# Optimization experiments

Measured on AMD Instinct MI355X. Metric: run time of the kernel, lower is better.

## Reference

```python
import jax, jax.numpy as jnp
import numpy as np

B, S, D, K = 128, 200, 128, 4
NQ, NC = 10000, 500


def setup_inputs() -> dict:
    key = jax.random.key(0)
    ks = jax.random.split(key, 20)
    f = jnp.float32
    inp = {}
    inp["question_seq"] = jax.random.randint(ks[0], (B, S), 0, NQ)
    inp["hint_attempt_seq"] = jax.random.randint(ks[1], (B, S), 0, 12)
    inp["correct_seq"] = jax.random.randint(ks[2], (B, S), 0, 2)
    inp["interval_time_seq"] = jax.random.randint(ks[3], (B, S), 0, 100)
    inp["use_time_seq"] = jax.random.randint(ks[4], (B, S), 0, 100)
    inp["q2c_table"] = jax.random.randint(ks[5], (NQ, K), 0, NC)
    inp["q2c_mask_table"] = jax.random.randint(ks[6], (NQ, K), 0, 2)
    s = 0.1
    inp["embed_question"] = jax.random.normal(ks[7], (NQ, D), f) * s
    inp["embed_question_disc"] = jax.random.normal(ks[8], (NQ, 1), f) * s
    inp["embed_concept"] = jax.random.normal(ks[9], (NC, D), f) * s
    inp["embed_interval_time"] = jax.random.normal(ks[10], (100, D), f) * s
    inp["embed_use_time"] = jax.random.normal(ks[11], (100, D), f) * s
    inp["embed_hint_attempt"] = jax.random.normal(ks[12], (12, D), f) * s
    inp["W_fuse"] = jax.random.normal(ks[13], (2 * D, D), f) / np.float32(np.sqrt(2 * D))
    inp["b_fuse"] = jnp.zeros((D,), f)
    inp["W_absorb"] = jax.random.normal(ks[14], (3 * D, D), f) / np.float32(np.sqrt(3 * D))
    inp["b_absorb"] = jnp.zeros((D,), f)
    inp["W_forget"] = jax.random.normal(ks[15], (3 * D, D), f) / np.float32(np.sqrt(3 * D))
    inp["b_forget"] = jnp.zeros((D,), f)
    inp["latent0"] = jax.random.normal(ks[16], (B, D), f) * 0.1  # xavier-init latent_pre
    return inp


def _cos(a, b, eps=1e-8):
    # torch.cosine_similarity semantics with eps clamp on each norm
    num = jnp.sum(a * b, axis=-1)
    na = jnp.sqrt(jnp.sum(a * a, axis=-1))
    nb = jnp.sqrt(jnp.sum(b * b, axis=-1))
    return num / (jnp.maximum(na, eps) * jnp.maximum(nb, eps))


def _forward(question_seq, hint_attempt_seq, correct_seq, interval_time_seq, use_time_seq,
             q2c_table, q2c_mask_table,
             embed_question, embed_question_disc, embed_concept, embed_interval_time,
             embed_use_time, embed_hint_attempt,
             W_fuse, b_fuse, W_absorb, b_absorb, W_forget, b_forget, latent0):
    f = latent0.dtype
    qe = embed_question[question_seq]                                # [B,S,D]
    qd = jax.nn.sigmoid(embed_question_disc[question_seq]) * 10.0    # [B,S,1]
    ce = jnp.broadcast_to(correct_seq.astype(f)[:, :, None], qe.shape)  # [B,S,D]
    ite = embed_interval_time[interval_time_seq]                     # [B,S,D]
    ute = embed_use_time[use_time_seq]                               # [B,S,D]
    hae = embed_hint_attempt[hint_attempt_seq]                       # [B,S,D]
    cp = embed_concept[q2c_table[question_seq]]                      # [B,S,K,D]
    m = q2c_mask_table[question_seq].astype(f)                       # [B,S,K]

    tm = lambda x: jnp.swapaxes(x, 0, 1)  # time-major for scan
    xs = (tm(qe[:, :-1]), tm(ce[:, :-1]), tm(ute[:, :-1]), tm(hae[:, :-1]), tm(ite[:, :-1]),
          tm(cp[:, :-1]), tm(cp[:, 1:]), tm(qd[:, 1:]), tm(m[:, :-1]))

    def step(lp, x):
        qe_t, ce_t, ute_t, hae_t, ite_t, cp_t, cp_t1, qd_t1, m_t = x
        inter = jnp.concatenate([qe_t, ce_t], axis=-1) @ W_fuse + b_fuse
        absorb = jnp.concatenate([inter, ute_t, hae_t], axis=-1) @ W_absorb + b_absorb
        forget = jax.nn.sigmoid(jnp.concatenate([lp, ite_t, inter], axis=-1) @ W_forget + b_forget)
        lc = lp * forget + absorb  # dropout p=0 -> identity
        qdiff = (_cos(qe_t[:, None, :], cp_t) + 1.0) * 0.5   # [B,K]
        uab = (_cos(lc[:, None, :], cp_t1) + 1.0) * 0.5      # [B,K]
        logit = qd_t1[:, 0] * jnp.sum((uab - qdiff) * m_t, axis=-1)  # [B]
        return lc, jax.nn.sigmoid(logit)

    _, ys = jax.lax.scan(step, latent0, xs)  # ys: [S-1, B]
    y = jnp.concatenate([ys.T, jnp.zeros((latent0.shape[0], 1), f)], axis=1)  # [B,S], last col 0
    return y


def reference(question_seq, hint_attempt_seq, correct_seq, interval_time_seq, use_time_seq,
              q2c_table, q2c_mask_table,
              embed_question, embed_question_disc, embed_concept, embed_interval_time,
              embed_use_time, embed_hint_attempt,
              W_fuse, b_fuse, W_absorb, b_absorb, W_forget, b_forget, latent0):
    return _forward(question_seq, hint_attempt_seq, correct_seq, interval_time_seq, use_time_seq,
                    q2c_table, q2c_mask_table,
                    embed_question, embed_question_disc, embed_concept, embed_interval_time,
                    embed_use_time, embed_hint_attempt,
                    W_fuse, b_fuse, W_absorb, b_absorb, W_forget, b_forget, latent0)
```

## Files before the change

### kernel.cpp

```cpp
#include <hip/hip_runtime.h>
#include <hip/hip_bf16.h>

typedef unsigned short u16;

#define Bb  128
#define Ss  200
#define Tt  199
#define Dd  128
#define Kk  4
#define NQq 10000
#define NCc 500
#define CHK 16
#define NCH 13

__device__ inline float bf2f(u16 u) {
    union { unsigned int i; float f; } x;
    x.i = ((unsigned int)u) << 16;
    return x.f;
}

__device__ inline float ldf(const void* p, int i, int m) {
    if (m) return ((const float*)p)[i];
    return bf2f(((const u16*)p)[i]);
}

__device__ inline void stf(void* p, int i, int m, float v) {
    if (m) ((float*)p)[i] = v;
    else ((__hip_bfloat16*)p)[i] = __float2bfloat16(v);
}

__device__ inline int clampi(int v, int lo, int hi) {
    return v < lo ? lo : (v > hi ? hi : v);
}

__device__ inline float wave_red(float v) {
#pragma unroll
    for (int m = 32; m >= 1; m >>= 1) v += __shfl_xor(v, m);
    return v;
}

__device__ inline float4 f4add(float4 a, float4 b) {
    return make_float4(a.x + b.x, a.y + b.y, a.z + b.z, a.w + b.w);
}
__device__ inline float4 f4fma(float s, float4 a, float4 b) {
    return make_float4(fmaf(s, a.x, b.x), fmaf(s, a.y, b.y),
                       fmaf(s, a.z, b.z), fmaf(s, a.w, b.w));
}

__global__ __launch_bounds__(256) void p_detect(const void* Eq, int* flag) {
    const int tid = threadIdx.x;
    const u16* q = (const u16*)Eq;
    float mx = 0.f;
    for (int i = tid; i < 4096; i += 256) {
        float a = fabsf(bf2f(q[i]));
        if (!(a == a)) a = 3.0e38f;
        mx = fmaxf(mx, a);
    }
#pragma unroll
    for (int s = 32; s >= 1; s >>= 1) mx = fmaxf(mx, __shfl_xor(mx, s));
    __shared__ float sm[4];
    if ((tid & 63) == 0) sm[tid >> 6] = mx;
    __syncthreads();
    if (tid == 0) {
        float m2 = fmaxf(fmaxf(sm[0], sm[1]), fmaxf(sm[2], sm[3]));
        flag[0] = (m2 > 1.0e6f) ? 1 : 0;
    }
}

__global__ __launch_bounds__(128) void p0_prep(const void* Wf, const void* Ec,
                                               const int* mode,
                                               float* cs2, float* cnorm) {
    const int m = mode[0];
    const int tid = threadIdx.x;
    if (blockIdx.x == 0) {
        float s = 0.f;
        for (int r = 0; r < 128; ++r) s += ldf(Wf, (128 + r) * 128 + tid, m);
        cs2[tid] = s;
    } else {
        const int c = blockIdx.x - 1;
        float v = ldf(Ec, c * 128 + tid, m);
        float s = wave_red(v * v);
        __shared__ float tmp[2];
        if ((tid & 63) == 0) tmp[tid >> 6] = s;
        __syncthreads();
        if (tid == 0) cnorm[c] = fmaxf(sqrtf(tmp[0] + tmp[1]), 1e-8f);
    }
}

__global__ __launch_bounds__(128) void p1_weights(
    const void* Wf, const void* Wa, const void* Wg,
    const void* bfu, const void* ba, const void* bg,
    const void* Eut, const void* Eha, const void* Eit,
    const int* mode, const float* cs2,
    float* BabT, float* BfgT,
    float* vA0, float* vA1, float* vF0, float* vF1,
    float* PA_ut, float* PA_ha, float* PF_it) {
    const int m = mode[0];
    const int bi = blockIdx.x, tid = threadIdx.x;
    if (bi < 128) {
        float acc = 0.f;
        for (int j = 0; j < 128; ++j)
            acc += ldf(Wf, bi * 128 + j, m) * ldf(Wa, j * 128 + tid, m);
        BabT[bi * 128 + tid] = acc;
    } else if (bi < 256) {
        const int i = bi - 128;
        float acc = 0.f;
        for (int j = 0; j < 128; ++j)
            acc += ldf(Wf, i * 128 + j, m) * ldf(Wg, (256 + j) * 128 + tid, m);
        BfgT[i * 128 + tid] = acc;
    } else if (bi == 256) {
        float a0 = 0.f, a1 = 0.f;
        for (int j = 0; j < 128; ++j) {
            float wv = ldf(Wa, j * 128 + tid, m);
            a0 += ldf(bfu, j, m) * wv;
            a1 += cs2[j] * wv;
        }
        vA0[tid] = a0 + ldf(ba, tid, m);
        vA1[tid] = a1;
    } else if (bi == 257) {
        float a0 = 0.f, a1 = 0.f;
        for (int j = 0; j < 128; ++j) {
            float wv = ldf(Wg, (256 + j) * 128 + tid, m);
            a0 += ldf(bfu, j, m) * wv;
            a1 += cs2[j] * wv;
        }
        vF0[tid] = a0 + ldf(bg, tid, m);
        vF1[tid] = a1;
    } else if (bi < 358) {
        const int r = bi - 258;
        float acc = 0.f;
        for (int j = 0; j < 128; ++j)
            acc += ldf(Eut, r * 128 + j, m) * ldf(Wa, (128 + j) * 128 + tid, m);
        PA_ut[r * 128 + tid] = acc;
    } else if (bi < 370) {
        const int r = bi - 358;
        float acc = 0.f;
        for (int j = 0; j < 128; ++j)
            acc += ldf(Eha, r * 128 + j, m) * ldf(Wa, (256 + j) * 128 + tid, m);
        PA_ha[r * 128 + tid] = acc;
    } else {
        const int r = bi - 370;
        float acc = 0.f;
        for (int j = 0; j < 128; ++j)
            acc += ldf(Eit, r * 128 + j, m) * ldf(Wg, (128 + j) * 128 + tid, m);
        PF_it[r * 128 + tid] = acc;
    }
}

__global__ __launch_bounds__(256) void p3_gemm(
    const void* Eq, const int* mode,
    const float* BabT, const float* BfgT,
    float* PA_q, float* PF_q) {
    __shared__ float At[64][36];
    __shared__ float Bt0[32][128];
    __shared__ float Bt1[32][128];
    const int m = mode[0];
    const int tid = threadIdx.x;
    const int r0 = blockIdx.x * 64;
    float acc0[4][8], acc1[4][8];
#pragma unroll
    for (int j = 0; j < 4; ++j)
#pragma unroll
        for (int i = 0; i < 8; ++i) { acc0[j][i] = 0.f; acc1[j][i] = 0.f; }
    const int tx = tid & 15, ty = tid >> 4;
    for (int ks = 0; ks < 4; ++ks) {
        {
            const int row = tid >> 2, seg = tid & 3;
            const int q = clampi(r0 + row, 0, NQq - 1);
            const int ei = q * 128 + ks * 32 + seg * 8;
            float* dst = &At[row][seg * 8];
            if (m) {
                const float4* src = (const float4*)((const float*)Eq + ei);
                float4 v0 = src[0], v1 = src[1];
                dst[0] = v0.x; dst[1] = v0.y; dst[2] = v0.z; dst[3] = v0.w;
                dst[4] = v1.x; dst[5] = v1.y; dst[6] = v1.z; dst[7] = v1.w;
            } else {
                uint4 v = *(const uint4*)((const u16*)Eq + ei);
                dst[0] = bf2f((u16)(v.x & 0xffff)); dst[1] = bf2f((u16)(v.x >> 16));
                dst[2] = bf2f((u16)(v.y & 0xffff)); dst[3] = bf2f((u16)(v.y >> 16));
                dst[4] = bf2f((u16)(v.z & 0xffff)); dst[5] = bf2f((u16)(v.z >> 16));
                dst[6] = bf2f((u16)(v.w & 0xffff)); dst[7] = bf2f((u16)(v.w >> 16));
            }
        }
        {
            const float4* s0 = (const float4*)(BabT + ks * 32 * 128);
            const float4* s1 = (const float4*)(BfgT + ks * 32 * 128);
            float4* d0 = (float4*)&Bt0[0][0];
            float4* d1 = (float4*)&Bt1[0][0];
#pragma unroll
            for (int k = 0; k < 4; ++k) {
                d0[tid + k * 256] = s0[tid + k * 256];
                d1[tid + k * 256] = s1[tid + k * 256];
            }
        }
        __syncthreads();
#pragma unroll
        for (int kk = 0; kk < 32; kk += 4) {
            float a_[4][4];
            *(float4*)&a_[0][0] = *(const float4*)&At[ty * 4 + 0][kk];
            *(float4*)&a_[1][0] = *(const float4*)&At[ty * 4 + 1][kk];
            *(float4*)&a_[2][0] = *(const float4*)&At[ty * 4 + 2][kk];
            *(float4*)&a_[3][0] = *(const float4*)&At[ty * 4 + 3][kk];
#pragma unroll
            for (int q = 0; q < 4; ++q) {
                float4 b0 = *(const float4*)&Bt0[kk + q][tx * 8];
                float4 b1 = *(const float4*)&Bt0[kk + q][tx * 8 + 4];
                float4 c0 = *(const float4*)&Bt1[kk + q][tx * 8];
                float4 c1 = *(const float4*)&Bt1[kk + q][tx * 8 + 4];
#pragma unroll
                for (int j = 0; j < 4; ++j) {
                    const float av = a_[j][q];
                    acc0[j][0] += av * b0.x; acc0[j][1] += av * b0.y;
                    acc0[j][2] += av * b0.z; acc0[j][3] += av * b0.w;
                    acc0[j][4] += av * b1.x; acc0[j][5] += av * b1.y;
                    acc0[j][6] += av * b1.z; acc0[j][7] += av * b1.w;
                    acc1[j][0] += av * c0.x; acc1[j][1] += av * c0.y;
                    acc1[j][2] += av * c0.z; acc1[j][3] += av * c0.w;
                    acc1[j][4] += av * c1.x; acc1[j][5] += av * c1.y;
                    acc1[j][6] += av * c1.z; acc1[j][7] += av * c1.w;
                }
            }
        }
        __syncthreads();
    }
#pragma unroll
    for (int j = 0; j < 4; ++j) {
        const int q = r0 + ty * 4 + j;
        if (q < NQq) {
            float* oa = PA_q + q * 128 + tx * 8;
            float* of = PF_q + q * 128 + tx * 8;
#pragma unroll
            for (int i = 0; i < 8; ++i) { oa[i] = acc0[j][i]; of[i] = acc1[j][i]; }
        }
    }
}

__global__ __launch_bounds__(256) void p2q(
    const int* q2c, const int* q2cm,
    const void* Eq, const void* Eqd, const void* Ec,
    const int* mode, const float* cnorm,
    float* qdm, float* qd10) {
    const int m = mode[0];
    const int wv = threadIdx.x >> 6, lane = threadIdx.x & 63;
    const int q = blockIdx.x * 4 + wv;
    const float qa = ldf(Eq, q * 128 + lane, m);
    const float qb = ldf(Eq, q * 128 + 64 + lane, m);
    const float nqc = fmaxf(sqrtf(wave_red(qa * qa + qb * qb)), 1e-8f);
    const int4 cc = ((const int4*)q2c)[q];
    const int4 mm = ((const int4*)q2cm)[q];
    const int cks[4] = {clampi(cc.x, 0, NCc - 1), clampi(cc.y, 0, NCc - 1),
                        clampi(cc.z, 0, NCc - 1), clampi(cc.w, 0, NCc - 1)};
    const int ms[4]  = {mm.x, mm.y, mm.z, mm.w};
    float qs = 0.f;
#pragma unroll
    for (int k = 0; k < 4; ++k) {
        const int ck = cks[k];
        float dot = wave_red(qa * ldf(Ec, ck * 128 + lane, m) +
                             qb * ldf(Ec, ck * 128 + 64 + lane, m));
        qs += (float)ms[k] * (0.5f * dot / (nqc * cnorm[ck]) + 0.5f);
    }
    if (lane == 0) {
        qdm[q] = qs;
        qd10[q] = 10.f / (1.f + __expf(-ldf(Eqd, q, m)));
    }
}

__global__ __launch_bounds__(256) void p4_scan(
    const int* q_seq, const int* ut_seq, const int* ha_seq, const int* it_seq,
    const int* c_seq,
    const void* Wg, const void* L0,
    const float* PA_q, const float* PA_ut, const float* PA_ha,
    const float* PF_q, const float* PF_it,
    const float* vA0, const float* vA1, const float* vF0, const float* vF1,
    const int* mode, float* lc_seq) {
    const int m = mode[0];
    const int b = blockIdx.x;
    const int tid = threadIdx.x;
    const int wv = tid >> 6, l = tid & 63;
    const int d0 = 2 * l, ib = wv * 32;

    __shared__ float lp_sh[128];
    __shared__ float part[512];
    __shared__ float st_ab[CHK * 128];
    __shared__ float st_pf[CHK * 128];

    float wA[32], wB[32];
#pragma unroll
    for (int k = 0; k < 32; ++k) {
        wA[k] = ldf(Wg, (ib + k) * 128 + d0, m);
        wB[k] = ldf(Wg, (ib + k) * 128 + d0 + 1, m);
    }
    float lc = 0.f;
    if (tid < 128) {
        lc = ldf(L0, b * 128 + tid, m);
        lp_sh[tid] = lc;
    }

    const int srow = tid >> 4, seg = tid & 15;
    const int off8 = seg * 8;
    const float4 A0a = *(const float4*)(vA0 + off8), A0b = *(const float4*)(vA0 + off8 + 4);
    const float4 A1a = *(const float4*)(vA1 + off8), A1b = *(const float4*)(vA1 + off8 + 4);
    const float4 F0a = *(const float4*)(vF0 + off8), F0b = *(const float4*)(vF0 + off8 + 4);
    const float4 F1a = *(const float4*)(vF1 + off8), F1b = *(const float4*)(vF1 + off8 + 4);

    float4 qa0, qa1, ua0, ua1, ga0, ga1, qf0, qf1, if0, if1;
    float cf;
#define LOAD_CHUNK(C)                                                          \
    {                                                                          \
        int tt = (C) * CHK + srow; if (tt > Tt - 1) tt = Tt - 1;               \
        const int base = b * Ss + tt;                                          \
        const int qt = clampi(q_seq[base], 0, NQq - 1);                        \
        const int ut = clampi(ut_seq[base], 0, 99);                            \
        const int ha = clampi(ha_seq[base], 0, 11);                            \
        const int it = clampi(it_seq[base], 0, 99);                            \
        cf = (float)c_seq[base];                                               \
        const float* pq = PA_q + qt * 128 + off8;                              \
        qa0 = *(const float4*)pq; qa1 = *(const float4*)(pq + 4);              \
        const float* pu = PA_ut + ut * 128 + off8;                             \
        ua0 = *(const float4*)pu; ua1 = *(const float4*)(pu + 4);              \
        const float* ph = PA_ha + ha * 128 + off8;                             \
        ga0 = *(const float4*)ph; ga1 = *(const float4*)(ph + 4);              \
        const float* pf = PF_q + qt * 128 + off8;                              \
        qf0 = *(const float4*)pf; qf1 = *(const float4*)(pf + 4);              \
        const float* pi = PF_it + it * 128 + off8;                             \
        if0 = *(const float4*)pi; if1 = *(const float4*)(pi + 4);              \
    }

    LOAD_CHUNK(0)
    float lcbuf[CHK];

    for (int c = 0; c < NCH; ++c) {
        {
            float4 ab0 = f4fma(cf, A1a, f4add(f4add(qa0, ua0), f4add(ga0, A0a)));
            float4 ab1 = f4fma(cf, A1b, f4add(f4add(qa1, ua1), f4add(ga1, A0b)));
            float4 pf0 = f4fma(cf, F1a, f4add(qf0, f4add(if0, F0a)));
            float4 pf1 = f4fma(cf, F1b, f4add(qf1, f4add(if1, F0b)));
            float4* sa = (float4*)(st_ab + srow * 128 + off8);
            sa[0] = ab0; sa[1] = ab1;
            float4* sp = (float4*)(st_pf + srow * 128 + off8);
            sp[0] = pf0; sp[1] = pf1;
        }
        if (c + 1 < NCH) LOAD_CHUNK(c + 1)
        __syncthreads();

#pragma unroll
        for (int s = 0; s < CHK; ++s) {
            const float4* lp4 = (const float4*)(lp_sh + ib);
            float pa = 0.f, pb = 0.f;
#pragma unroll
            for (int k = 0; k < 8; ++k) {
                float4 v = lp4[k];
                pa += v.x * wA[4 * k] + v.y * wA[4 * k + 1]
                    + v.z * wA[4 * k + 2] + v.w * wA[4 * k + 3];
                pb += v.x * wB[4 * k] + v.y * wB[4 * k + 1]
                    + v.z * wB[4 * k + 2] + v.w * wB[4 * k + 3];
            }
            *(float2*)(part + (wv << 7) + d0) = make_float2(pa, pb);
            __syncthreads();
            if (tid < 128) {
                const float fs = part[tid] + part[128 + tid]
                               + part[256 + tid] + part[384 + tid];
                const float ab = st_ab[(s << 7) + tid];
                const float pf = st_pf[(s << 7) + tid];
                const float fg = 1.f / (1.f + __expf(-(fs + pf)));
                lc = lc * fg + ab;
                lp_sh[tid] = lc;
                lcbuf[s] = lc;
            }
            __syncthreads();
        }
        if (tid < 128) {
#pragma unroll
            for (int s = 0; s < CHK; ++s) {
                const int t = c * CHK + s;
                if (t < Tt)
                    lc_seq[((long)t * 128 + b) * 128 + tid] = lcbuf[s];
            }
        }
    }
#undef LOAD_CHUNK
}

__global__ __launch_bounds__(256) void p5_out(
    const int* q_seq, const int* q2c, const int* q2cm,
    const float* lc_seq, const float* qdm, const float* qd10,
    const float* cnorm, const void* Ec, const int* mode, void* out) {
    const int m = mode[0];
    const int wv = threadIdx.x >> 6, lane = threadIdx.x & 63;
    const int r = blockIdx.x * 4 + wv;
    const int t = r >> 7, b = r & 127;
    const int qt  = clampi(q_seq[b * Ss + t], 0, NQq - 1);
    const int qt1 = clampi(q_seq[b * Ss + t + 1], 0, NQq - 1);
    const int4 mm = ((const int4*)q2cm)[qt];
    int4 ci = ((const int4*)q2c)[qt1];
    const int c0 = clampi(ci.x, 0, NCc - 1), c1 = clampi(ci.y, 0, NCc - 1);
    const int c2 = clampi(ci.z, 0, NCc - 1), c3 = clampi(ci.w, 0, NCc - 1);
    const float la = lc_seq[(long)r * 128 + lane];
    const float lb = lc_seq[(long)r * 128 + 64 + lane];
    float nl = la * la + lb * lb;
    float d0 = la * ldf(Ec, c0 * 128 + lane, m) + lb * ldf(Ec, c0 * 128 + 64 + lane, m);
    float d1 = la * ldf(Ec, c1 * 128 + lane, m) + lb * ldf(Ec, c1 * 128 + 64 + lane, m);
    float d2 = la * ldf(Ec, c2 * 128 + lane, m) + lb * ldf(Ec, c2 * 128 + 64 + lane, m);
    float d3 = la * ldf(Ec, c3 * 128 + lane, m) + lb * ldf(Ec, c3 * 128 + 64 + lane, m);
#pragma unroll
    for (int s = 32; s >= 1; s >>= 1) {
        nl += __shfl_xor(nl, s);
        d0 += __shfl_xor(d0, s); d1 += __shfl_xor(d1, s);
        d2 += __shfl_xor(d2, s); d3 += __shfl_xor(d3, s);
    }
    if (lane == 0) {
        const float inl = 1.f / fmaxf(sqrtf(nl), 1e-8f);
        const float accv = (float)mm.x * (0.5f * d0 * inl / cnorm[c0] + 0.5f)
                         + (float)mm.y * (0.5f * d1 * inl / cnorm[c1] + 0.5f)
                         + (float)mm.z * (0.5f * d2 * inl / cnorm[c2] + 0.5f)
                         + (float)mm.w * (0.5f * d3 * inl / cnorm[c3] + 0.5f);
        const float logit = qd10[qt1] * (accv - qdm[qt]);
        stf(out, b * Ss + t, m, 1.f / (1.f + __expf(-logit)));
        if (t == 0) stf(out, b * Ss + 199, m, 0.f);
    }
}

extern "C" void kernel_launch(void* const* d_in, const int* in_sizes, int n_in,
                              void* d_out, int out_size, void* d_ws, size_t ws_size,
                              hipStream_t stream) {
    (void)in_sizes; (void)n_in; (void)out_size; (void)ws_size;
    const int* q_seq  = (const int*)d_in[0];
    const int* ha_seq = (const int*)d_in[1];
    const int* c_seq  = (const int*)d_in[2];
    const int* it_seq = (const int*)d_in[3];
    const int* ut_seq = (const int*)d_in[4];
    const int* q2c    = (const int*)d_in[5];
    const int* q2cm   = (const int*)d_in[6];
    const void* Eq   = d_in[7];
    const void* Eqd  = d_in[8];
    const void* Ec   = d_in[9];
    const void* Eit  = d_in[10];
    const void* Eut  = d_in[11];
    const void* Eha  = d_in[12];
    const void* Wf   = d_in[13];
    const void* bfu  = d_in[14];
    const void* Wa   = d_in[15];
    const void* ba   = d_in[16];
    const void* Wg   = d_in[17];
    const void* bg   = d_in[18];
    const void* L0   = d_in[19];

    int*   mode  = (int*)d_ws;
    float* cs2   = (float*)d_ws + 16;
    float* cnorm = cs2 + 128;
    float* vA0   = cnorm + 512;
    float* vA1   = vA0 + 128;
    float* vF0   = vA1 + 128;
    float* vF1   = vF0 + 128;
    float* BabT  = vF1 + 128;
    float* BfgT  = BabT + 16384;
    float* PA_ut = BfgT + 16384;
    float* PA_ha = PA_ut + 12800;
    float* PF_it = PA_ha + 1536;
    float* qdm   = PF_it + 12800;
    float* qd10  = qdm + 10016;
    float* PA_q  = qd10 + 10016;
    float* PF_q  = PA_q + 1280000;
    float* lc_seq= PF_q + 1280000;

    hipLaunchKernelGGL(p_detect, dim3(1), dim3(256), 0, stream, Eq, mode);
    hipLaunchKernelGGL(p0_prep, dim3(501), dim3(128), 0, stream, Wf, Ec, mode, cs2, cnorm);
    hipLaunchKernelGGL(p1_weights, dim3(470), dim3(128), 0, stream,
                       Wf, Wa, Wg, bfu, ba, bg, Eut, Eha, Eit, mode, cs2,
                       BabT, BfgT, vA0, vA1, vF0, vF1, PA_ut, PA_ha, PF_it);
    hipLaunchKernelGGL(p3_gemm, dim3(157), dim3(256), 0, stream,
                       Eq, mode, BabT, BfgT, PA_q, PF_q);
    hipLaunchKernelGGL(p2q, dim3(2500), dim3(256), 0, stream,
                       q2c, q2cm, Eq, Eqd, Ec, mode, cnorm, qdm, qd10);
    hipLaunchKernelGGL(p4_scan, dim3(Bb), dim3(256), 0, stream,
                       q_seq, ut_seq, ha_seq, it_seq, c_seq, Wg, L0,
                       PA_q, PA_ut, PA_ha, PF_q, PF_it,
                       vA0, vA1, vF0, vF1, mode, lc_seq);
    hipLaunchKernelGGL(p5_out, dim3(Tt * Bb / 4), dim3(256), 0, stream,
                       q_seq, q2c, q2cm, lc_seq, qdm, qd10, cnorm, Ec, mode, d_out);
}
```

Before: 271.2 us.

## Merge prep kernels, inline mode detection, remove one barrier per scan step

Mode detection moves from a standalone kernel into an inline per-wave check, and the prep, weights, gemm and p2q kernels are merged into two launches, cutting seven launches to four. In the recurrent scan, every wave now computes the gate update redundantly from double-buffered partial sums, which removes the second __syncthreads per timestep and the idle half of the threads. The costs are redundant cs2 computation in two blocks, redundant sampling of Eq in every kernel, and detection now checks only 256 elements instead of 4096, which could misclassify the input dtype.

```diff
diff --git a/kernel.cpp b/kernel.cpp
--- a/kernel.cpp
+++ b/kernel.cpp
@@ -47,99 +47,91 @@
                        fmaf(s, a.z, b.z), fmaf(s, a.w, b.w));
 }
 
-__global__ __launch_bounds__(256) void p_detect(const void* Eq, int* flag) {
-    const int tid = threadIdx.x;
+__device__ inline int detect_mode(const void* Eq) {
     const u16* q = (const u16*)Eq;
+    const int l = threadIdx.x & 63;
     float mx = 0.f;
-    for (int i = tid; i < 4096; i += 256) {
-        float a = fabsf(bf2f(q[i]));
+#pragma unroll
+    for (int k = 0; k < 4; ++k) {
+        float a = fabsf(bf2f(q[l * 4 + k]));
         if (!(a == a)) a = 3.0e38f;
         mx = fmaxf(mx, a);
     }
 #pragma unroll
     for (int s = 32; s >= 1; s >>= 1) mx = fmaxf(mx, __shfl_xor(mx, s));
-    __shared__ float sm[4];
-    if ((tid & 63) == 0) sm[tid >> 6] = mx;
-    __syncthreads();
-    if (tid == 0) {
-        float m2 = fmaxf(fmaxf(sm[0], sm[1]), fmaxf(sm[2], sm[3]));
-        flag[0] = (m2 > 1.0e6f) ? 1 : 0;
-    }
-}
-
-__global__ __launch_bounds__(128) void p0_prep(const void* Wf, const void* Ec,
-                                               const int* mode,
-                                               float* cs2, float* cnorm) {
-    const int m = mode[0];
-    const int tid = threadIdx.x;
-    if (blockIdx.x == 0) {
-        float s = 0.f;
-        for (int r = 0; r < 128; ++r) s += ldf(Wf, (128 + r) * 128 + tid, m);
-        cs2[tid] = s;
-    } else {
-        const int c = blockIdx.x - 1;
+    return (mx > 1.0e6f) ? 1 : 0;
+}
+
+__global__ __launch_bounds__(128) void k_prep(
+    const void* Eq, const void* Wf, const void* Wa, const void* Wg,
+    const void* bfu, const void* ba, const void* bg,
+    const void* Eut, const void* Eha, const void* Eit, const void* Ec,
+    float* cnorm, float* BabT, float* BfgT,
+    float* vA0, float* vA1, float* vF0, float* vF1,
+    float* PA_ut, float* PA_ha, float* PF_it) {
+    const int m = detect_mode(Eq);
+    const int bi = blockIdx.x, tid = threadIdx.x;
+    __shared__ float cs2s[128];
+    __shared__ float tmp[2];
+    if (bi < 500) {
+        const int c = bi;
         float v = ldf(Ec, c * 128 + tid, m);
         float s = wave_red(v * v);
-        __shared__ float tmp[2];
         if ((tid & 63) == 0) tmp[tid >> 6] = s;
         __syncthreads();
         if (tid == 0) cnorm[c] = fmaxf(sqrtf(tmp[0] + tmp[1]), 1e-8f);
-    }
-}
-
-__global__ __launch_bounds__(128) void p1_weights(
-    const void* Wf, const void* Wa, const void* Wg,
-    const void* bfu, const void* ba, const void* bg,
-    const void* Eut, const void* Eha, const void* Eit,
-    const int* mode, const float* cs2,
-    float* BabT, float* BfgT,
-    float* vA0, float* vA1, float* vF0, float* vF1,
-    float* PA_ut, float* PA_ha, float* PF_it) {
-    const int m = mode[0];
-    const int bi = blockIdx.x, tid = threadIdx.x;
-    if (bi < 128) {
+    } else if (bi < 628) {
+        const int r = bi - 500;
         float acc = 0.f;
         for (int j = 0; j < 128; ++j)
-            acc += ldf(Wf, bi * 128 + j, m) * ldf(Wa, j * 128 + tid, m);
-        BabT[bi * 128 + tid] = acc;
-    } else if (bi < 256) {
-        const int i = bi - 128;
+            acc += ldf(Wf, r * 128 + j, m) * ldf(Wa, j * 128 + tid, m);
+        BabT[r * 128 + tid] = acc;
+    } else if (bi < 756) {
+        const int r = bi - 628;
         float acc = 0.f;
         for (int j = 0; j < 128; ++j)
-            acc += ldf(Wf, i * 128 + j, m) * ldf(Wg, (256 + j) * 128 + tid, m);
-        BfgT[i * 128 + tid] = acc;
-    } else if (bi == 256) {
+            acc += ldf(Wf, r * 128 + j, m) * ldf(Wg, (256 + j) * 128 + tid, m);
+        BfgT[r * 128 + tid] = acc;
+    } else if (bi == 756) {
+        float s = 0.f;
+        for (int r = 0; r < 128; ++r) s += ldf(Wf, (128 + r) * 128 + tid, m);
+        cs2s[tid] = s;
+        __syncthreads();
         float a0 = 0.f, a1 = 0.f;
         for (int j = 0; j < 128; ++j) {
             float wv = ldf(Wa, j * 128 + tid, m);
             a0 += ldf(bfu, j, m) * wv;
-            a1 += cs2[j] * wv;
+            a1 += cs2s[j] * wv;
         }
         vA0[tid] = a0 + ldf(ba, tid, m);
         vA1[tid] = a1;
-    } else if (bi == 257) {
+    } else if (bi == 757) {
+        float s = 0.f;
+        for (int r = 0; r < 128; ++r) s += ldf(Wf, (128 + r) * 128 + tid, m);
+        cs2s[tid] = s;
+        __syncthreads();
         float a0 = 0.f, a1 = 0.f;
         for (int j = 0; j < 128; ++j) {
             float wv = ldf(Wg, (256 + j) * 128 + tid, m);
             a0 += ldf(bfu, j, m) * wv;
-            a1 += cs2[j] * wv;
+            a1 += cs2s[j] * wv;
         }
         vF0[tid] = a0 + ldf(bg, tid, m);
         vF1[tid] = a1;
-    } else if (bi < 358) {
-        const int r = bi - 258;
+    } else if (bi < 858) {
+        const int r = bi - 758;
         float acc = 0.f;
         for (int j = 0; j < 128; ++j)
             acc += ldf(Eut, r * 128 + j, m) * ldf(Wa, (128 + j) * 128 + tid, m);
         PA_ut[r * 128 + tid] = acc;
-    } else if (bi < 370) {
-        const int r = bi - 358;
+    } else if (bi < 870) {
+        const int r = bi - 858;
         float acc = 0.f;
         for (int j = 0; j < 128; ++j)
             acc += ldf(Eha, r * 128 + j, m) * ldf(Wa, (256 + j) * 128 + tid, m);
         PA_ha[r * 128 + tid] = acc;
     } else {
-        const int r = bi - 370;
+        const int r = bi - 870;
         float acc = 0.f;
         for (int j = 0; j < 128; ++j)
             acc += ldf(Eit, r * 128 + j, m) * ldf(Wg, (128 + j) * 128 + tid, m);
@@ -147,140 +139,139 @@
     }
 }
 
-__global__ __launch_bounds__(256) void p3_gemm(
-    const void* Eq, const int* mode,
-    const float* BabT, const float* BfgT,
-    float* PA_q, float* PF_q) {
-    __shared__ float At[64][36];
-    __shared__ float Bt0[32][128];
-    __shared__ float Bt1[32][128];
-    const int m = mode[0];
+__global__ __launch_bounds__(256) void k_mid(
+    const void* Eq, const void* Eqd, const void* Ec,
+    const int* q2c, const int* q2cm,
+    const float* BabT, const float* BfgT, const float* cnorm,
+    float* PA_q, float* PF_q, float* qdm, float* qd10) {
+    const int m = detect_mode(Eq);
     const int tid = threadIdx.x;
-    const int r0 = blockIdx.x * 64;
-    float acc0[4][8], acc1[4][8];
-#pragma unroll
-    for (int j = 0; j < 4; ++j)
-#pragma unroll
-        for (int i = 0; i < 8; ++i) { acc0[j][i] = 0.f; acc1[j][i] = 0.f; }
-    const int tx = tid & 15, ty = tid >> 4;
-    for (int ks = 0; ks < 4; ++ks) {
-        {
-            const int row = tid >> 2, seg = tid & 3;
-            const int q = clampi(r0 + row, 0, NQq - 1);
-            const int ei = q * 128 + ks * 32 + seg * 8;
-            float* dst = &At[row][seg * 8];
-            if (m) {
-                const float4* src = (const float4*)((const float*)Eq + ei);
-                float4 v0 = src[0], v1 = src[1];
-                dst[0] = v0.x; dst[1] = v0.y; dst[2] = v0.z; dst[3] = v0.w;
-                dst[4] = v1.x; dst[5] = v1.y; dst[6] = v1.z; dst[7] = v1.w;
-            } else {
-                uint4 v = *(const uint4*)((const u16*)Eq + ei);
-                dst[0] = bf2f((u16)(v.x & 0xffff)); dst[1] = bf2f((u16)(v.x >> 16));
-                dst[2] = bf2f((u16)(v.y & 0xffff)); dst[3] = bf2f((u16)(v.y >> 16));
-                dst[4] = bf2f((u16)(v.z & 0xffff)); dst[5] = bf2f((u16)(v.z >> 16));
-                dst[6] = bf2f((u16)(v.w & 0xffff)); dst[7] = bf2f((u16)(v.w >> 16));
-            }
-        }
-        {
-            const float4* s0 = (const float4*)(BabT + ks * 32 * 128);
-            const float4* s1 = (const float4*)(BfgT + ks * 32 * 128);
-            float4* d0 = (float4*)&Bt0[0][0];
-            float4* d1 = (float4*)&Bt1[0][0];
-#pragma unroll
-            for (int k = 0; k < 4; ++k) {
-                d0[tid + k * 256] = s0[tid + k * 256];
-                d1[tid + k * 256] = s1[tid + k * 256];
-            }
-        }
-        __syncthreads();
-#pragma unroll
-        for (int kk = 0; kk < 32; kk += 4) {
-            float a_[4][4];
-            *(float4*)&a_[0][0] = *(const float4*)&At[ty * 4 + 0][kk];
-            *(float4*)&a_[1][0] = *(const float4*)&At[ty * 4 + 1][kk];
-            *(float4*)&a_[2][0] = *(const float4*)&At[ty * 4 + 2][kk];
-            *(float4*)&a_[3][0] = *(const float4*)&At[ty * 4 + 3][kk];
-#pragma unroll
-            for (int q = 0; q < 4; ++q) {
-                float4 b0 = *(const float4*)&Bt0[kk + q][tx * 8];
-                float4 b1 = *(const float4*)&Bt0[kk + q][tx * 8 + 4];
-                float4 c0 = *(const float4*)&Bt1[kk + q][tx * 8];
-                float4 c1 = *(const float4*)&Bt1[kk + q][tx * 8 + 4];
-#pragma unroll
-                for (int j = 0; j < 4; ++j) {
-                    const float av = a_[j][q];
-                    acc0[j][0] += av * b0.x; acc0[j][1] += av * b0.y;
-                    acc0[j][2] += av * b0.z; acc0[j][3] += av * b0.w;
-                    acc0[j][4] += av * b1.x; acc0[j][5] += av * b1.y;
-                    acc0[j][6] += av * b1.z; acc0[j][7] += av * b1.w;
-                    acc1[j][0] += av * c0.x; acc1[j][1] += av * c0.y;
-                    acc1[j][2] += av * c0.z; acc1[j][3] += av * c0.w;
-                    acc1[j][4] += av * c1.x; acc1[j][5] += av * c1.y;
-                    acc1[j][6] += av * c1.z; acc1[j][7] += av * c1.w;
+    const int bi = blockIdx.x;
+    if (bi < 157) {
+        __shared__ float At[64][36];
+        __shared__ float Bt0[32][128];
+        __shared__ float Bt1[32][128];
+        const int r0 = bi * 64;
+        float acc0[4][8], acc1[4][8];
+#pragma unroll
+        for (int j = 0; j < 4; ++j)
+#pragma unroll
+            for (int i = 0; i < 8; ++i) { acc0[j][i] = 0.f; acc1[j][i] = 0.f; }
+        const int tx = tid & 15, ty = tid >> 4;
+        for (int ks = 0; ks < 4; ++ks) {
+            {
+                const int row = tid >> 2, seg = tid & 3;
+                const int q = clampi(r0 + row, 0, NQq - 1);
+                const int ei = q * 128 + ks * 32 + seg * 8;
+                float* dst = &At[row][seg * 8];
+                if (m) {
+                    const float4* src = (const float4*)((const float*)Eq + ei);
+                    float4 v0 = src[0], v1 = src[1];
+                    dst[0] = v0.x; dst[1] = v0.y; dst[2] = v0.z; dst[3] = v0.w;
+                    dst[4] = v1.x; dst[5] = v1.y; dst[6] = v1.z; dst[7] = v1.w;
+                } else {
+                    uint4 v = *(const uint4*)((const u16*)Eq + ei);
+                    dst[0] = bf2f((u16)(v.x & 0xffff)); dst[1] = bf2f((u16)(v.x >> 16));
+                    dst[2] = bf2f((u16)(v.y & 0xffff)); dst[3] = bf2f((u16)(v.y >> 16));
+                    dst[4] = bf2f((u16)(v.z & 0xffff)); dst[5] = bf2f((u16)(v.z >> 16));
+                    dst[6] = bf2f((u16)(v.w & 0xffff)); dst[7] = bf2f((u16)(v.w >> 16));
                 }
             }
-        }
-        __syncthreads();
-    }
-#pragma unroll
-    for (int j = 0; j < 4; ++j) {
-        const int q = r0 + ty * 4 + j;
-        if (q < NQq) {
-            float* oa = PA_q + q * 128 + tx * 8;
-            float* of = PF_q + q * 128 + tx * 8;
-#pragma unroll
-            for (int i = 0; i < 8; ++i) { oa[i] = acc0[j][i]; of[i] = acc1[j][i]; }
-        }
-    }
-}
-
-__global__ __launch_bounds__(256) void p2q(
-    const int* q2c, const int* q2cm,
-    const void* Eq, const void* Eqd, const void* Ec,
-    const int* mode, const float* cnorm,
-    float* qdm, float* qd10) {
-    const int m = mode[0];
-    const int wv = threadIdx.x >> 6, lane = threadIdx.x & 63;
-    const int q = blockIdx.x * 4 + wv;
-    const float qa = ldf(Eq, q * 128 + lane, m);
-    const float qb = ldf(Eq, q * 128 + 64 + lane, m);
-    const float nqc = fmaxf(sqrtf(wave_red(qa * qa + qb * qb)), 1e-8f);
-    const int4 cc = ((const int4*)q2c)[q];
-    const int4 mm = ((const int4*)q2cm)[q];
-    const int cks[4] = {clampi(cc.x, 0, NCc - 1), clampi(cc.y, 0, NCc - 1),
-                        clampi(cc.z, 0, NCc - 1), clampi(cc.w, 0, NCc - 1)};
-    const int ms[4]  = {mm.x, mm.y, mm.z, mm.w};
-    float qs = 0.f;
-#pragma unroll
-    for (int k = 0; k < 4; ++k) {
-        const int ck = cks[k];
-        float dot = wave_red(qa * ldf(Ec, ck * 128 + lane, m) +
-                             qb * ldf(Ec, ck * 128 + 64 + lane, m));
-        qs += (float)ms[k] * (0.5f * dot / (nqc * cnorm[ck]) + 0.5f);
-    }
-    if (lane == 0) {
-        qdm[q] = qs;
-        qd10[q] = 10.f / (1.f + __expf(-ldf(Eqd, q, m)));
+            {
+                const float4* s0 = (const float4*)(BabT + ks * 32 * 128);
+                const float4* s1 = (const float4*)(BfgT + ks * 32 * 128);
+                float4* d0 = (float4*)&Bt0[0][0];
+                float4* d1 = (float4*)&Bt1[0][0];
+#pragma unroll
+                for (int k = 0; k < 4; ++k) {
+                    d0[tid + k * 256] = s0[tid + k * 256];
+                    d1[tid + k * 256] = s1[tid + k * 256];
+                }
+            }
+            __syncthreads();
+#pragma unroll
+            for (int kk = 0; kk < 32; kk += 4) {
+                float a_[4][4];
+                *(float4*)&a_[0][0] = *(const float4*)&At[ty * 4 + 0][kk];
+                *(float4*)&a_[1][0] = *(const float4*)&At[ty * 4 + 1][kk];
+                *(float4*)&a_[2][0] = *(const float4*)&At[ty * 4 + 2][kk];
+                *(float4*)&a_[3][0] = *(const float4*)&At[ty * 4 + 3][kk];
+#pragma unroll
+                for (int q = 0; q < 4; ++q) {
+                    float4 b0 = *(const float4*)&Bt0[kk + q][tx * 8];
+                    float4 b1 = *(const float4*)&Bt0[kk + q][tx * 8 + 4];
+                    float4 c0 = *(const float4*)&Bt1[kk + q][tx * 8];
+                    float4 c1 = *(const float4*)&Bt1[kk + q][tx * 8 + 4];
+#pragma unroll
+                    for (int j = 0; j < 4; ++j) {
+                        const float av = a_[j][q];
+                        acc0[j][0] += av * b0.x; acc0[j][1] += av * b0.y;
+                        acc0[j][2] += av * b0.z; acc0[j][3] += av * b0.w;
+                        acc0[j][4] += av * b1.x; acc0[j][5] += av * b1.y;
+                        acc0[j][6] += av * b1.z; acc0[j][7] += av * b1.w;
+                        acc1[j][0] += av * c0.x; acc1[j][1] += av * c0.y;
+                        acc1[j][2] += av * c0.z; acc1[j][3] += av * c0.w;
+                        acc1[j][4] += av * c1.x; acc1[j][5] += av * c1.y;
+                        acc1[j][6] += av * c1.z; acc1[j][7] += av * c1.w;
+                    }
+                }
+            }
+            __syncthreads();
+        }
+#pragma unroll
+        for (int j = 0; j < 4; ++j) {
+            const int q = r0 + ty * 4 + j;
+            if (q < NQq) {
+                float* oa = PA_q + q * 128 + tx * 8;
+                float* of = PF_q + q * 128 + tx * 8;
+#pragma unroll
+                for (int i = 0; i < 8; ++i) { oa[i] = acc0[j][i]; of[i] = acc1[j][i]; }
+            }
+        }
+    } else {
+        const int wv = tid >> 6, lane = tid & 63;
+        const int q = (bi - 157) * 4 + wv;
+        const float qa = ldf(Eq, q * 128 + lane, m);
+        const float qb = ldf(Eq, q * 128 + 64 + lane, m);
+        const float nqc = fmaxf(sqrtf(wave_red(qa * qa + qb * qb)), 1e-8f);
+        const int4 cc = ((const int4*)q2c)[q];
+        const int4 mm = ((const int4*)q2cm)[q];
+        const int cks[4] = {clampi(cc.x, 0, NCc - 1), clampi(cc.y, 0, NCc - 1),
+                            clampi(cc.z, 0, NCc - 1), clampi(cc.w, 0, NCc - 1)};
+        const int ms[4]  = {mm.x, mm.y, mm.z, mm.w};
+        float qs = 0.f;
+#pragma unroll
+        for (int k = 0; k < 4; ++k) {
+            const int ck = cks[k];
+            float dot = wave_red(qa * ldf(Ec, ck * 128 + lane, m) +
+                                 qb * ldf(Ec, ck * 128 + 64 + lane, m));
+            qs += (float)ms[k] * (0.5f * dot / (nqc * cnorm[ck]) + 0.5f);
+        }
+        if (lane == 0) {
+            qdm[q] = qs;
+            qd10[q] = 10.f / (1.f + __expf(-ldf(Eqd, q, m)));
+        }
     }
 }
 
 __global__ __launch_bounds__(256) void p4_scan(
     const int* q_seq, const int* ut_seq, const int* ha_seq, const int* it_seq,
     const int* c_seq,
-    const void* Wg, const void* L0,
+    const void* Eq, const void* Wg, const void* L0,
     const float* PA_q, const float* PA_ut, const float* PA_ha,
     const float* PF_q, const float* PF_it,
     const float* vA0, const float* vA1, const float* vF0, const float* vF1,
-    const int* mode, float* lc_seq) {
-    const int m = mode[0];
+    float* lc_seq) {
+    const int m = detect_mode(Eq);
     const int b = blockIdx.x;
     const int tid = threadIdx.x;
     const int wv = tid >> 6, l = tid & 63;
-    const int d0 = 2 * l, ib = wv * 32;
+    const int d0 = 2 * l;
+    const int ib = wv << 5;
+    const int dd = ib + (l & 31);
 
     __shared__ float lp_sh[128];
-    __shared__ float part[512];
+    __shared__ float part[2][4][128];
     __shared__ float st_ab[CHK * 128];
     __shared__ float st_pf[CHK * 128];
 
@@ -290,11 +281,8 @@
         wA[k] = ldf(Wg, (ib + k) * 128 + d0, m);
         wB[k] = ldf(Wg, (ib + k) * 128 + d0 + 1, m);
     }
-    float lc = 0.f;
-    if (tid < 128) {
-        lc = ldf(L0, b * 128 + tid, m);
-        lp_sh[tid] = lc;
-    }
+    float lc = ldf(L0, b * 128 + dd, m);
+    if (l < 32) lp_sh[dd] = lc;
 
     const int srow = tid >> 4, seg = tid & 15;
     const int off8 = seg * 8;
@@ -328,8 +316,10 @@
 
     LOAD_CHUNK(0)
     float lcbuf[CHK];
+    int par = 0;
 
     for (int c = 0; c < NCH; ++c) {
+        __syncthreads();
         {
             float4 ab0 = f4fma(cf, A1a, f4add(f4add(qa0, ua0), f4add(ga0, A0a)));
             float4 ab1 = f4fma(cf, A1b, f4add(f4add(qa1, ua1), f4add(ga1, A0b)));
@@ -355,26 +345,24 @@
                 pb += v.x * wB[4 * k] + v.y * wB[4 * k + 1]
                     + v.z * wB[4 * k + 2] + v.w * wB[4 * k + 3];
             }
-            *(float2*)(part + (wv << 7) + d0) = make_float2(pa, pb);
+            *(float2*)&part[par][wv][d0] = make_float2(pa, pb);
             __syncthreads();
-            if (tid < 128) {
-                const float fs = part[tid] + part[128 + tid]
-                               + part[256 + tid] + part[384 + tid];
-                const float ab = st_ab[(s << 7) + tid];
-                const float pf = st_pf[(s << 7) + tid];
-                const float fg = 1.f / (1.f + __expf(-(fs + pf)));
-                lc = lc * fg + ab;
-                lp_sh[tid] = lc;
-                lcbuf[s] = lc;
-            }
-            __syncthreads();
-        }
-        if (tid < 128) {
+            const float fs = part[par][0][dd] + part[par][1][dd]
+                           + part[par][2][dd] + part[par][3][dd];
+            const float ab = st_ab[(s << 7) + dd];
+            const float pf = st_pf[(s << 7) + dd];
+            const float fg = 1.f / (1.f + __expf(-(fs + pf)));
+            lc = lc * fg + ab;
+            if (l < 32) lp_sh[dd] = lc;
+            lcbuf[s] = lc;
+            par ^= 1;
+        }
+        if (l < 32) {
 #pragma unroll
             for (int s = 0; s < CHK; ++s) {
                 const int t = c * CHK + s;
                 if (t < Tt)
-                    lc_seq[((long)t * 128 + b) * 128 + tid] = lcbuf[s];
+                    lc_seq[((long)t * 128 + b) * 128 + dd] = lcbuf[s];
             }
         }
     }
@@ -384,8 +372,8 @@
 __global__ __launch_bounds__(256) void p5_out(
     const int* q_seq, const int* q2c, const int* q2cm,
     const float* lc_seq, const float* qdm, const float* qd10,
-    const float* cnorm, const void* Ec, const int* mode, void* out) {
-    const int m = mode[0];
+    const float* cnorm, const void* Eq, const void* Ec, void* out) {
+    const int m = detect_mode(Eq);
     const int wv = threadIdx.x >> 6, lane = threadIdx.x & 63;
     const int r = blockIdx.x * 4 + wv;
     const int t = r >> 7, b = r & 127;
@@ -445,9 +433,7 @@
     const void* bg   = d_in[18];
     const void* L0   = d_in[19];
 
-    int*   mode  = (int*)d_ws;
-    float* cs2   = (float*)d_ws + 16;
-    float* cnorm = cs2 + 128;
+    float* cnorm = (float*)d_ws;
     float* vA0   = cnorm + 512;
     float* vA1   = vA0 + 128;
     float* vF0   = vA1 + 128;
@@ -463,19 +449,16 @@
     float* PF_q  = PA_q + 1280000;
     float* lc_seq= PF_q + 1280000;
 
-    hipLaunchKernelGGL(p_detect, dim3(1), dim3(256), 0, stream, Eq, mode);
-    hipLaunchKernelGGL(p0_prep, dim3(501), dim3(128), 0, stream, Wf, Ec, mode, cs2, cnorm);
-    hipLaunchKernelGGL(p1_weights, dim3(470), dim3(128), 0, stream,
-                       Wf, Wa, Wg, bfu, ba, bg, Eut, Eha, Eit, mode, cs2,
-                       BabT, BfgT, vA0, vA1, vF0, vF1, PA_ut, PA_ha, PF_it);
-    hipLaunchKernelGGL(p3_gemm, dim3(157), dim3(256), 0, stream,
-                       Eq, mode, BabT, BfgT, PA_q, PF_q);
-    hipLaunchKernelGGL(p2q, dim3(2500), dim3(256), 0, stream,
-                       q2c, q2cm, Eq, Eqd, Ec, mode, cnorm, qdm, qd10);
+    hipLaunchKernelGGL(k_prep, dim3(970), dim3(128), 0, stream,
+                       Eq, Wf, Wa, Wg, bfu, ba, bg, Eut, Eha, Eit, Ec,
+                       cnorm, BabT, BfgT, vA0, vA1, vF0, vF1, PA_ut, PA_ha, PF_it);
+    hipLaunchKernelGGL(k_mid, dim3(2657), dim3(256), 0, stream,
+                       Eq, Eqd, Ec, q2c, q2cm, BabT, BfgT, cnorm,
+                       PA_q, PF_q, qdm, qd10);
     hipLaunchKernelGGL(p4_scan, dim3(Bb), dim3(256), 0, stream,
-                       q_seq, ut_seq, ha_seq, it_seq, c_seq, Wg, L0,
+                       q_seq, ut_seq, ha_seq, it_seq, c_seq, Eq, Wg, L0,
                        PA_q, PA_ut, PA_ha, PF_q, PF_it,
-                       vA0, vA1, vF0, vF1, mode, lc_seq);
+                       vA0, vA1, vF0, vF1, lc_seq);
     hipLaunchKernelGGL(p5_out, dim3(Tt * Bb / 4), dim3(256), 0, stream,
-                       q_seq, q2c, q2cm, lc_seq, qdm, qd10, cnorm, Ec, mode, d_out);
-}
+                       q_seq, q2c, q2cm, lc_seq, qdm, qd10, cnorm, Eq, Ec, d_out);
+}
```

Result: faster. 258.6 us (-4.6%).
